# Optimization experiments

Measured on AMD Instinct MI355X. Metric: run time of the kernel, lower is better.

## Reference

```python
import jax, jax.numpy as jnp
import numpy as np

N_HIDDEN = 512
N_MEMORY = 128
BUDGET = 16
BATCH = 32768


def setup_inputs() -> dict:
    key = jax.random.key(0)
    ks = jax.random.split(key, 4)
    s1 = 1.0 / np.sqrt(N_HIDDEN + N_MEMORY)
    s2 = 1.0 / np.sqrt(2048)
    return {
        "x": jax.random.normal(ks[0], (BATCH, N_HIDDEN), dtype=jnp.float32),
        "W1": jax.random.normal(ks[1], (N_HIDDEN + N_MEMORY, 2048), dtype=jnp.float32) * s1,
        "b1": jnp.zeros((2048,), dtype=jnp.float32),
        "W2": jax.random.normal(ks[2], (2048, 2048), dtype=jnp.float32) * s2,
        "b2": jnp.zeros((2048,), dtype=jnp.float32),
        "W3": jax.random.normal(ks[3], (2048, N_HIDDEN + N_MEMORY + 2), dtype=jnp.float32) * s2,
        "b3": jnp.zeros((N_HIDDEN + N_MEMORY + 2,), dtype=jnp.float32),
    }


def reference(x, W1, b1, W2, b2, W3, b3):
    batch = x.shape[0]
    dtype = x.dtype

    memory = jnp.zeros((batch, N_MEMORY), dtype=dtype).at[:, 0].set(float(BUDGET))
    halted = jnp.zeros((batch,), dtype=bool)
    final_probs = jnp.zeros((batch,), dtype=dtype)
    n_iters = jnp.zeros((batch,), dtype=dtype)  # never updated in the original forward

    def mlp(inp):
        h = jax.nn.relu(inp @ W1 + b1)
        h = jax.nn.relu(h @ W2 + b2)
        return h @ W3 + b3

    def step(carry, _):
        x, mem, halted, fp = carry
        out = mlp(jnp.concatenate([x, mem], axis=-1))  # [B, 2+H+M]
        probs = out[:, 0]
        halt_val = out[:, 1]
        hidden_out = out[:, 2:2 + N_HIDDEN]
        mem_out = out[:, 2 + N_HIDDEN:]
        active = ~halted
        # torch compacts with boolean masks; masked-where is the dense equivalent
        x = jnp.where(active[:, None], hidden_out, x)
        mem = jnp.where(active[:, None], mem_out, mem)
        halt = jax.nn.sigmoid(halt_val) > 0.5  # sigmoid().round().bool()
        newly = active & halt
        fp = jnp.where(newly, probs, fp)
        halted = halted | newly
        return (x, mem, halted, fp), None

    (x, memory, halted, final_probs), _ = jax.lax.scan(
        step, (x, memory, halted, final_probs), None, length=BUDGET)

    return jax.nn.sigmoid(final_probs), n_iters
```

## Files before the change

### kernel.cpp

```cpp
#include <hip/hip_runtime.h>
#include <math.h>

typedef _Float16 f16;
typedef _Float16 f16x8 __attribute__((ext_vector_type(8)));
typedef float f32x4 __attribute__((ext_vector_type(4)));

#define NB 32768
#define NH 512
#define NM 128
#define NIN 640
#define NHID 2048
#define NOUT 642
#define NOUTP 768
#define ITERS 16
#define S1 2048.0f
#define EPS1 4.8828125e-4f

__device__ __forceinline__ void gload16(const void* g, void* lds) {
  __builtin_amdgcn_global_load_lds(
      reinterpret_cast<const __attribute__((address_space(1))) unsigned int*>((uintptr_t)g),
      reinterpret_cast<__attribute__((address_space(3))) unsigned int*>((unsigned int)(uintptr_t)lds),
      16, 0, 0);
}

__device__ __forceinline__ f32x4 mfma16(f16x8 a, f16x8 b, f32x4 c) {
  return __builtin_amdgcn_mfma_f32_16x16x32_f16(a, b, c, 0, 0, 0);
}

__device__ __forceinline__ void split2(float v, f16& a0, f16& a1) {
  a0 = (f16)v;
  a1 = (f16)((v - (float)a0) * S1);
}

__global__ void k_prepW(const float* __restrict__ W, f16* __restrict__ WT,
                        int K, int Nreal) {
  __shared__ float tile[32][33];
  int k0 = blockIdx.x * 32, n0 = blockIdx.y * 32;
  int tx = threadIdx.x & 31, ty = threadIdx.x >> 5;
#pragma unroll
  for (int r = 0; r < 4; ++r) {
    int kk = ty + 8 * r;
    int n = n0 + tx;
    tile[kk][tx] = (n < Nreal) ? W[(size_t)(k0 + kk) * Nreal + n] : 0.0f;
  }
  __syncthreads();
#pragma unroll
  for (int r = 0; r < 4; ++r) {
    int nl = ty + 8 * r;
    float v = tile[tx][nl];
    f16 a0, a1; split2(v, a0, a1);
    size_t o = (size_t)(n0 + nl) * (2 * K) + k0 + tx;
    WT[o] = a0; WT[o + K] = a1;
  }
}

__global__ void k_splitX(const float* __restrict__ x, f16* __restrict__ xm2) {
  int i = blockIdx.x * 256 + threadIdx.x;
  int row = i >> 9, c = i & 511;
  f16 a0, a1; split2(x[i], a0, a1);
  size_t o = (size_t)row * (2 * NIN) + c;
  xm2[o] = a0; xm2[o + NIN] = a1;
}

__global__ void k_init(f16* __restrict__ xm2, float* __restrict__ fpb,
                       int* __restrict__ list0, int* __restrict__ cnt) {
  int gid = blockIdx.x * blockDim.x + threadIdx.x;
  if (gid < NB * NM) {
    int row = gid >> 7, c = gid & 127;
    size_t o = (size_t)row * (2 * NIN) + 512 + c;
    xm2[o] = (f16)((c == 0) ? 16.0f : 0.0f);
    xm2[o + NIN] = (f16)0.0f;
  }
  if (gid < NB) { fpb[gid] = 0.0f; list0[gid] = gid; }
  if (gid < 32) cnt[gid] = (gid == 0) ? NB : 0;
}


#define GEMM_PREAMBLE()                                                     \
  int tid = threadIdx.x;                                                    \
  int w = tid >> 6, lane = tid & 63;                                        \
  int wr = w >> 1, wc = w & 1;                                              \
  int lm = lane & 15, kb = lane >> 4;                                       \
  int kidx = ((kb ^ ((lm >> 1) & 3)) << 3);                                 \
  int ksrc = (((tid & 3) ^ ((tid >> 3) & 3)) << 3);                         \
  int stg = tid * 8;                                                        \
  int afo[4], bfo[4];                                                       \
  _Pragma("unroll") for (int m = 0; m < 4; ++m)                             \
    afo[m] = (wr * 64 + m * 16 + lm) * 32 + kidx;                           \
  _Pragma("unroll") for (int n = 0; n < 4; ++n)                             \
    bfo[n] = (wc * 64 + n * 16 + lm) * 32 + kidx + 8192;                    \
  f32x4 acc0[4][4], acc1[4][4];                                             \
  _Pragma("unroll") for (int m = 0; m < 4; ++m)                             \
  _Pragma("unroll") for (int n = 0; n < 4; ++n) {                           \
    acc0[m][n] = (f32x4)0.0f; acc1[m][n] = (f32x4)0.0f;                     \
  }

#define GEMM_COMPUTE(BASE)                                                  \
  {                                                                         \
    const f16* _sb = (BASE);                                                \
    f16x8 fa0[4], fa1[4], fb0[4], fb1[4];                                   \
    _Pragma("unroll") for (int m = 0; m < 4; ++m) {                         \
      fa0[m] = *(const f16x8*)&_sb[afo[m]];                                 \
      fa1[m] = *(const f16x8*)&_sb[4096 + afo[m]];                          \
    }                                                                       \
    _Pragma("unroll") for (int n = 0; n < 4; ++n) {                         \
      fb0[n] = *(const f16x8*)&_sb[bfo[n]];                                 \
      fb1[n] = *(const f16x8*)&_sb[4096 + bfo[n]];                          \
    }                                                                       \
    __builtin_amdgcn_s_setprio(1);                                          \
    _Pragma("unroll") for (int m = 0; m < 4; ++m)                           \
    _Pragma("unroll") for (int n = 0; n < 4; ++n) {                         \
      acc0[m][n] = mfma16(fa0[m], fb0[n], acc0[m][n]);                      \
      acc1[m][n] = mfma16(fa0[m], fb1[n], acc1[m][n]);                      \
      acc1[m][n] = mfma16(fa1[m], fb0[n], acc1[m][n]);                      \
    }                                                                       \
    __builtin_amdgcn_s_setprio(0);                                          \
  }

#define STAGE8(K0, DST, PSA, PSB)                                           \
  {                                                                         \
    _Pragma("unroll") for (int s = 0; s < 2; ++s) {                         \
      gload16(pA + s * (PSA) + (K0), (DST) + s * 4096 + stg);               \
      gload16(pA2 + s * (PSA) + (K0), (DST) + 2048 + s * 4096 + stg);       \
    }                                                                       \
    _Pragma("unroll") for (int s = 0; s < 2; ++s) {                         \
      gload16(pB + s * (PSB) + (K0), (DST) + 8192 + s * 4096 + stg);        \
      gload16(pB2 + s * (PSB) + (K0), (DST) + 10240 + s * 4096 + stg);      \
    }                                                                       \
  }

#define GEMM_PIPELOOP(KTOT, PSA, PSB)                                       \
  STAGE8(0, &SB[0], PSA, PSB);                                              \
  __syncthreads();                                                          \
  {                                                                         \
    int pb = 0;                                                             \
    for (int k0 = 0; k0 < (KTOT); k0 += 32, pb ^= 1) {                      \
      if (k0 + 32 < (KTOT))                                                 \
        STAGE8(k0 + 32, pb ? &SB[0] : &SB[16384], PSA, PSB);                \
      GEMM_COMPUTE(pb ? &SB[16384] : &SB[0]);                               \
      __syncthreads();                                                      \
    }                                                                       \
  }

#define COMBINE(m, n, q) (acc0[m][n][q] + EPS1 * acc1[m][n][q])

#define MAP16(ID, BX, NY) int NY = ((ID) & 7) + 8 * (((ID) >> 3) & 1); int BX = (ID) >> 4;

__global__ __launch_bounds__(256, 2) void k_l1(
    const f16* __restrict__ xm2, const f16* __restrict__ WT,
    const float* __restrict__ b1, f16* __restrict__ h1,
    const int* __restrict__ list, const int* __restrict__ cntp,
    int chunk_off, int chunk_rows) {
  int cnt = *cntp;
  MAP16(blockIdx.x, bx, ny);
  int lm0 = bx * 128;
  if (chunk_off + lm0 >= cnt) return;
  int lim = cnt - chunk_off; if (lim > chunk_rows) lim = chunk_rows;
  int n0 = ny * 128;

  __shared__ f16 SB[2 * 16384];
  GEMM_PREAMBLE();

  int pu = chunk_off + lm0 + (tid >> 2);
  int pu2 = pu + 64;
  int idx = list[pu < cnt ? pu : (cnt - 1)];
  int idx2 = list[pu2 < cnt ? pu2 : (cnt - 1)];
  const f16* pA = xm2 + (size_t)idx * (2 * NIN) + ksrc;
  const f16* pA2 = xm2 + (size_t)idx2 * (2 * NIN) + ksrc;
  const f16* pB = WT + (size_t)(n0 + (tid >> 2)) * (2 * NIN) + ksrc;
  const f16* pB2 = pB + (size_t)64 * (2 * NIN);

  GEMM_PIPELOOP(NIN, NIN, NIN);

#pragma unroll
  for (int n = 0; n < 4; ++n) {
    int col = n0 + wc * 64 + n * 16 + lm;
    float bb = b1[col];
#pragma unroll
    for (int m = 0; m < 4; ++m) {
#pragma unroll
      for (int q = 0; q < 4; ++q) {
        int gr = lm0 + wr * 64 + m * 16 + kb * 4 + q;
        if (gr < lim) {
          float v = fmaxf(COMBINE(m, n, q) + bb, 0.0f);
          f16 a0, a1; split2(v, a0, a1);
          size_t o = (size_t)gr * (2 * NHID) + col;
          h1[o] = a0; h1[o + NHID] = a1;
        }
      }
    }
  }
}

__global__ __launch_bounds__(256, 2) void k_l2(
    const f16* __restrict__ h1, const f16* __restrict__ WT,
    const float* __restrict__ b2, f16* __restrict__ h2,
    const int* __restrict__ cntp, int chunk_off, int chunk_rows) {
  int cnt = *cntp;
  MAP16(blockIdx.x, bx, ny);
  int lm0 = bx * 128;
  if (chunk_off + lm0 >= cnt) return;
  int lim = cnt - chunk_off; if (lim > chunk_rows) lim = chunk_rows;
  int n0 = ny * 128;

  __shared__ f16 SB[2 * 16384];
  GEMM_PREAMBLE();

  const f16* pA = h1 + (size_t)(lm0 + (tid >> 2)) * (2 * NHID) + ksrc;
  const f16* pA2 = pA + (size_t)64 * (2 * NHID);
  const f16* pB = WT + (size_t)(n0 + (tid >> 2)) * (2 * NHID) + ksrc;
  const f16* pB2 = pB + (size_t)64 * (2 * NHID);

  GEMM_PIPELOOP(NHID, NHID, NHID);

#pragma unroll
  for (int n = 0; n < 4; ++n) {
    int col = n0 + wc * 64 + n * 16 + lm;
    float bb = b2[col];
#pragma unroll
    for (int m = 0; m < 4; ++m) {
#pragma unroll
      for (int q = 0; q < 4; ++q) {
        int gr = lm0 + wr * 64 + m * 16 + kb * 4 + q;
        if (gr < lim) {
          float v = fmaxf(COMBINE(m, n, q) + bb, 0.0f);
          f16 a0, a1; split2(v, a0, a1);
          size_t o = (size_t)gr * (2 * NHID) + col;
          h2[o] = a0; h2[o + NHID] = a1;
        }
      }
    }
  }
}

__global__ __launch_bounds__(256, 2) void k_l3(
    const f16* __restrict__ h2, const f16* __restrict__ WT,
    const float* __restrict__ b3, f16* __restrict__ xm2,
    float* __restrict__ probs, float* __restrict__ hv,
    const int* __restrict__ list, const int* __restrict__ cntp,
    int chunk_off, int chunk_rows) {
  int cnt = *cntp;
  int id = blockIdx.x;
  int bx = id / 6, ny = id - bx * 6;
  int lm0 = bx * 128;
  if (chunk_off + lm0 >= cnt) return;
  int lim = cnt - chunk_off; if (lim > chunk_rows) lim = chunk_rows;
  int n0 = ny * 128;

  __shared__ f16 SB[2 * 16384];
  GEMM_PREAMBLE();

  const f16* pA = h2 + (size_t)(lm0 + (tid >> 2)) * (2 * NHID) + ksrc;
  const f16* pA2 = pA + (size_t)64 * (2 * NHID);
  const f16* pB = WT + (size_t)(n0 + (tid >> 2)) * (2 * NHID) + ksrc;
  const f16* pB2 = pB + (size_t)64 * (2 * NHID);

  GEMM_PIPELOOP(NHID, NHID, NHID);

  float bb[4]; int colv[4];
#pragma unroll
  for (int n = 0; n < 4; ++n) {
    colv[n] = n0 + wc * 64 + n * 16 + lm;
    bb[n] = (colv[n] < NOUT) ? b3[colv[n]] : 0.0f;
  }
#pragma unroll
  for (int m = 0; m < 4; ++m) {
#pragma unroll
    for (int q = 0; q < 4; ++q) {
      int gr = lm0 + wr * 64 + m * 16 + kb * 4 + q;
      if (gr >= lim) continue;
      int r = list[chunk_off + gr];
#pragma unroll
      for (int n = 0; n < 4; ++n) {
        int col = colv[n];
        if (col >= NOUT) continue;
        float v = COMBINE(m, n, q) + bb[n];
        if (col == 0) {
          probs[r] = v;
        } else if (col == 1) {
          hv[r] = v;
        } else if (col < 2 + NH) {
          f16 a0, a1; split2(v, a0, a1);
          size_t o = (size_t)r * (2 * NIN) + (col - 2);
          xm2[o] = a0; xm2[o + NIN] = a1;
        } else {
          f16 a0, a1; split2(v, a0, a1);
          size_t o = (size_t)r * (2 * NIN) + 512 + (col - 2 - NH);
          xm2[o] = a0; xm2[o + NIN] = a1;
        }
      }
    }
  }
}

__global__ void k_update(const int* __restrict__ listc, int* __restrict__ listn,
                         const float* __restrict__ hv, const float* __restrict__ probs,
                         float* __restrict__ fpb, const int* __restrict__ cntc,
                         int* __restrict__ cntn) {
  int i = blockIdx.x * blockDim.x + threadIdx.x;
  if (i >= *cntc) return;
  int r = listc[i];
  if (hv[r] > 0.0f) {
    fpb[r] = probs[r];
  } else {
    int pos = atomicAdd(cntn, 1);
    listn[pos] = r;
  }
}

__global__ void k_final(const float* __restrict__ fpb, float* __restrict__ out) {
  int i = blockIdx.x * blockDim.x + threadIdx.x;
  if (i < NB) {
    out[i] = 1.0f / (1.0f + expf(-fpb[i]));
    out[NB + i] = 0.0f;
  }
}

extern "C" void kernel_launch(void* const* d_in, const int* in_sizes, int n_in,
                              void* d_out, int out_size, void* d_ws, size_t ws_size,
                              hipStream_t stream) {
  const float* x  = (const float*)d_in[0];
  const float* W1 = (const float*)d_in[1];
  const float* b1 = (const float*)d_in[2];
  const float* W2 = (const float*)d_in[3];
  const float* b2 = (const float*)d_in[4];
  const float* W3 = (const float*)d_in[5];
  const float* b3 = (const float*)d_in[6];
  float* out = (float*)d_out;

  char* p = (char*)d_ws;
  auto alloc = [&](size_t bytes) {
    char* r = p;
    p += (bytes + 255) & ~(size_t)255;
    return r;
  };
  f16* xm2  = (f16*)alloc((size_t)NB * 2 * NIN * 2);
  f16* W1T  = (f16*)alloc((size_t)NHID * 2 * NIN * 2);
  f16* W2T  = (f16*)alloc((size_t)NHID * 2 * NHID * 2);
  f16* W3T  = (f16*)alloc((size_t)NOUTP * 2 * NHID * 2);
  float* probs = (float*)alloc((size_t)NB * 4);
  float* hvb   = (float*)alloc((size_t)NB * 4);
  float* fpb   = (float*)alloc((size_t)NB * 4);
  int* list0   = (int*)alloc((size_t)NB * 4);
  int* list1   = (int*)alloc((size_t)NB * 4);
  int* cnt     = (int*)alloc(32 * 4);

  size_t used = (size_t)(p - (char*)d_ws);
  size_t remain = (ws_size > used) ? (ws_size - used) : 0;
  long long chl = (long long)(remain / ((size_t)2 * 2 * NHID * 2));
  int CH = (int)(chl > NB ? NB : chl);
  CH &= ~127;
  if (CH < 128) CH = 128;
  f16* h1 = (f16*)alloc((size_t)CH * 2 * NHID * 2);
  f16* h2 = (f16*)alloc((size_t)CH * 2 * NHID * 2);
  int nchunks = (NB + CH - 1) / CH;

  k_prepW<<<dim3(NIN / 32, NHID / 32), 256, 0, stream>>>(W1, W1T, NIN, NHID);
  k_prepW<<<dim3(NHID / 32, NHID / 32), 256, 0, stream>>>(W2, W2T, NHID, NHID);
  k_prepW<<<dim3(NHID / 32, NOUTP / 32), 256, 0, stream>>>(W3, W3T, NHID, NOUT);
  k_splitX<<<(NB * NH) / 256, 256, 0, stream>>>(x, xm2);
  k_init<<<(NB * NM) / 256, 256, 0, stream>>>(xm2, fpb, list0, cnt);

  for (int t = 0; t < ITERS; ++t) {
    const int* lc = (t & 1) ? list1 : list0;
    int* ln       = (t & 1) ? list0 : list1;
    const int* cc = cnt + t;
    int* cn       = cnt + t + 1;
    for (int c = 0; c < nchunks; ++c) {
      int off = c * CH;
      int rows = NB - off; if (rows > CH) rows = CH;
      int g1 = (CH / 128) * 16;
      k_l1<<<g1, 256, 0, stream>>>(xm2, W1T, b1, h1, lc, cc, off, rows);
      k_l2<<<g1, 256, 0, stream>>>(h1, W2T, b2, h2, cc, off, rows);
      int g3 = (CH / 128) * 6;
      k_l3<<<g3, 256, 0, stream>>>(h2, W3T, b3, xm2, probs, hvb, lc, cc, off, rows);
    }
    k_update<<<NB / 256, 256, 0, stream>>>(lc, ln, hvb, probs, fpb, cc, cn);
  }
  k_final<<<NB / 256, 256, 0, stream>>>(fpb, out);
}
```

Measured before the change: 3.993 ms.

## Fuse halt/update step into layer-3 epilogue and cap chunk size

```diff
diff --git a/kernel.cpp b/kernel.cpp
--- a/kernel.cpp
+++ b/kernel.cpp
@@ -236,8 +236,9 @@
 __global__ __launch_bounds__(256, 2) void k_l3(
     const f16* __restrict__ h2, const f16* __restrict__ WT,
     const float* __restrict__ b3, f16* __restrict__ xm2,
-    float* __restrict__ probs, float* __restrict__ hv,
-    const int* __restrict__ list, const int* __restrict__ cntp,
+    float* __restrict__ fpb,
+    const int* __restrict__ list, int* __restrict__ listn,
+    const int* __restrict__ cntp, int* __restrict__ cntn,
     int chunk_off, int chunk_rows) {
   int cnt = *cntp;
   int id = blockIdx.x;
@@ -257,6 +258,9 @@
 
   GEMM_PIPELOOP(NHID, NHID, NHID);
 
+  float* SBp = (float*)SB;
+  float* SBh = (float*)SB + 128;
+
   float bb[4]; int colv[4];
 #pragma unroll
   for (int n = 0; n < 4; ++n) {
@@ -276,9 +280,9 @@
         if (col >= NOUT) continue;
         float v = COMBINE(m, n, q) + bb[n];
         if (col == 0) {
-          probs[r] = v;
+          SBp[gr - lm0] = v;
         } else if (col == 1) {
-          hv[r] = v;
+          SBh[gr - lm0] = v;
         } else if (col < 2 + NH) {
           f16 a0, a1; split2(v, a0, a1);
           size_t o = (size_t)r * (2 * NIN) + (col - 2);
@@ -291,20 +295,19 @@
       }
     }
   }
-}
-
-__global__ void k_update(const int* __restrict__ listc, int* __restrict__ listn,
-                         const float* __restrict__ hv, const float* __restrict__ probs,
-                         float* __restrict__ fpb, const int* __restrict__ cntc,
-                         int* __restrict__ cntn) {
-  int i = blockIdx.x * blockDim.x + threadIdx.x;
-  if (i >= *cntc) return;
-  int r = listc[i];
-  if (hv[r] > 0.0f) {
-    fpb[r] = probs[r];
-  } else {
-    int pos = atomicAdd(cntn, 1);
-    listn[pos] = r;
+
+  if (ny == 0) {
+    __syncthreads();
+    int rcount = lim - lm0; if (rcount > 128) rcount = 128;
+    if (tid < rcount) {
+      int r = list[chunk_off + lm0 + tid];
+      if (SBh[tid] > 0.0f) {
+        fpb[r] = SBp[tid];
+      } else {
+        int pos = atomicAdd(cntn, 1);
+        listn[pos] = r;
+      }
+    }
   }
 }
 
@@ -338,8 +341,6 @@
   f16* W1T  = (f16*)alloc((size_t)NHID * 2 * NIN * 2);
   f16* W2T  = (f16*)alloc((size_t)NHID * 2 * NHID * 2);
   f16* W3T  = (f16*)alloc((size_t)NOUTP * 2 * NHID * 2);
-  float* probs = (float*)alloc((size_t)NB * 4);
-  float* hvb   = (float*)alloc((size_t)NB * 4);
   float* fpb   = (float*)alloc((size_t)NB * 4);
   int* list0   = (int*)alloc((size_t)NB * 4);
   int* list1   = (int*)alloc((size_t)NB * 4);
@@ -350,6 +351,7 @@
   long long chl = (long long)(remain / ((size_t)2 * 2 * NHID * 2));
   int CH = (int)(chl > NB ? NB : chl);
   CH &= ~127;
+  if (CH > 8192) CH = 8192;
   if (CH < 128) CH = 128;
   f16* h1 = (f16*)alloc((size_t)CH * 2 * NHID * 2);
   f16* h2 = (f16*)alloc((size_t)CH * 2 * NHID * 2);
@@ -373,9 +375,8 @@
       k_l1<<<g1, 256, 0, stream>>>(xm2, W1T, b1, h1, lc, cc, off, rows);
       k_l2<<<g1, 256, 0, stream>>>(h1, W2T, b2, h2, cc, off, rows);
       int g3 = (CH / 128) * 6;
-      k_l3<<<g3, 256, 0, stream>>>(h2, W3T, b3, xm2, probs, hvb, lc, cc, off, rows);
-    }
-    k_update<<<NB / 256, 256, 0, stream>>>(lc, ln, hvb, probs, fpb, cc, cn);
+      k_l3<<<g3, 256, 0, stream>>>(h2, W3T, b3, xm2, fpb, lc, ln, cc, cn, off, rows);
+    }
   }
   k_final<<<NB / 256, 256, 0, stream>>>(fpb, out);
 }
```

Measured after the change: 3.879 ms (median of 2 runs). 1.03x faster.
